# Performance work log

Hardware: AMD Instinct MI355X
Metric: run time of the kernel (lower is better)

The kernel has to match this reference:

```python
import jax, jax.numpy as jnp
import numpy as np
from jax import lax

BN_EPS = 1e-5
HEADS = 2


def dw_conv(x, w, stride, pad):
    # depthwise conv, NCHW, weight OIHW with I=1, groups=C
    return lax.conv_general_dilated(
        x, w, (stride, stride), [(pad, pad), (pad, pad)],
        dimension_numbers=('NCHW', 'OIHW', 'NCHW'),
        feature_group_count=x.shape[1])


def bn(x, g, b, m, v):
    inv = g * lax.rsqrt(v + BN_EPS)
    return (x - m[:, None, None]) * inv[:, None, None] + b[:, None, None]


def conv1x1(x, w, b):
    return jnp.einsum('bchw,oc->bohw', x, w) + b[:, None, None]


def setup_inputs() -> dict:
    key = jax.random.key(0)
    ks = jax.random.split(key, 20)
    B, C, H, W = 32, 128, 56, 56
    r = lambda i, shape, s=0.05: jax.random.normal(ks[i], shape, jnp.float32) * s
    return {
        'x': jax.random.normal(ks[0], (B, C, H, W), jnp.float32),
        'q_w': r(1, (C, C)), 'q_b': r(2, (C,)),
        'kv_w': r(3, (2 * C, C)), 'kv_b': r(4, (2 * C,)),
        'sr1_w': r(5, (C, 1, 4, 4), 0.2),
        'sr1_g': jax.random.uniform(ks[6], (C,), jnp.float32) + 0.5,
        'sr1_b': r(7, (C,)),
        'sr1_m': r(8, (C,)),
        'sr1_v': jax.random.uniform(ks[9], (C,), jnp.float32) + 0.5,
        'sr2_w': r(10, (C, 1, 1, 1), 0.5),
        'sr2_g': jax.random.uniform(ks[11], (C,), jnp.float32) + 0.5,
        'sr2_b': r(12, (C,)),
        'sr2_m': r(13, (C,)),
        'sr2_v': jax.random.uniform(ks[14], (C,), jnp.float32) + 0.5,
        'local_w': r(15, (C, 1, 3, 3), 0.2), 'local_b': r(16, (C,)),
    }


def reference(x, q_w, q_b, kv_w, kv_b,
              sr1_w, sr1_g, sr1_b, sr1_m, sr1_v,
              sr2_w, sr2_g, sr2_b, sr2_m, sr2_v,
              local_w, local_b):
    B, C, H, W = x.shape
    h = HEADS
    d = C // h
    scale = d ** -0.5

    # q projection: 1x1 conv -> [B, h, N, d]
    q = conv1x1(x, q_w, q_b)
    q = q.reshape(B, h, d, H * W).transpose(0, 1, 3, 2)

    # spatial reduction: depthwise strided conv + BN + ReLU, then depthwise 1x1 + BN
    kv = jax.nn.relu(bn(dw_conv(x, sr1_w, 4, 2), sr1_g, sr1_b, sr1_m, sr1_v))
    kv = bn(kv * sr2_w.reshape(C, 1, 1), sr2_g, sr2_b, sr2_m, sr2_v)

    # depthwise 3x3 local conv + residual
    kv = dw_conv(kv, local_w, 1, 1) + local_b[:, None, None] + kv

    # kv projection and split
    kvp = conv1x1(kv, kv_w, kv_b)
    k, v = jnp.split(kvp, 2, axis=1)
    Nk = k.shape[2] * k.shape[3]
    k = k.reshape(B, h, d, Nk)                       # [B,h,d,Nk]
    v = v.reshape(B, h, d, Nk).transpose(0, 1, 3, 2)  # [B,h,Nk,d]

    attn = jax.nn.softmax(jnp.einsum('bhnd,bhdm->bhnm', q, k) * scale, axis=-1)
    out = jnp.einsum('bhnm,bhmd->bhnd', attn, v)      # [B,h,N,d]
    return out.transpose(0, 1, 3, 2).reshape(B, C, H, W)
```

## Files before the change

kernel.cpp:

```cpp
#include <hip/hip_runtime.h>
#include <hip/hip_bf16.h>

#define B_    32
#define C_    128
#define H_    56
#define W_    56
#define N_    3136
#define HK_   15
#define NK_   225
#define D_    64

typedef __attribute__((ext_vector_type(8))) short bf16x8;
typedef __attribute__((ext_vector_type(4))) float f32x4;

__device__ __forceinline__ float b2f(unsigned short u) {
    union { float f; unsigned int i; } x;
    x.i = ((unsigned int)u) << 16;
    return x.f;
}
__device__ __forceinline__ unsigned short f2b(float f) {
    __hip_bfloat16 h = __float2bfloat16(f);
    return *(unsigned short*)&h;
}

__device__ __forceinline__ void gll16(const char* g, char* l) {
    __builtin_amdgcn_global_load_lds(
        (const __attribute__((address_space(1))) unsigned int*)g,
        (__attribute__((address_space(3))) unsigned int*)l,
        16, 0, 0);
}

__global__ __launch_bounds__(256) void srlocal_kernel(
        const float* __restrict__ x,
        const float* __restrict__ sr1_w, const float* __restrict__ sr1_g,
        const float* __restrict__ sr1_b, const float* __restrict__ sr1_m,
        const float* __restrict__ sr1_v, const float* __restrict__ sr2_w,
        const float* __restrict__ sr2_g, const float* __restrict__ sr2_b,
        const float* __restrict__ sr2_m, const float* __restrict__ sr2_v,
        const float* __restrict__ local_w, const float* __restrict__ local_b,
        float* __restrict__ kv2) {
    int bc = blockIdx.x;
    int c  = bc & (C_ - 1);
    int tid = threadIdx.x;
    __shared__ float xim[H_ * W_];
    __shared__ float kvt[HK_][HK_ + 1];

    const float* xp = x + (size_t)bc * (H_ * W_);
    for (int idx = tid; idx < (H_ * W_) / 4; idx += 256)
        ((float4*)xim)[idx] = ((const float4*)xp)[idx];
    __syncthreads();

    int p = tid;
    int oy = p / HK_, ox = p % HK_;
    if (p < NK_) {
        float s = 0.f;
#pragma unroll
        for (int ky = 0; ky < 4; ++ky) {
            int iy = oy * 4 - 2 + ky;
            if (iy < 0 || iy >= H_) continue;
#pragma unroll
            for (int kx = 0; kx < 4; ++kx) {
                int ix = ox * 4 - 2 + kx;
                if (ix < 0 || ix >= W_) continue;
                s += xim[iy * W_ + ix] * sr1_w[c * 16 + ky * 4 + kx];
            }
        }
        float inv1 = sr1_g[c] * rsqrtf(sr1_v[c] + 1e-5f);
        s = (s - sr1_m[c]) * inv1 + sr1_b[c];
        s = fmaxf(s, 0.f);
        s *= sr2_w[c];
        float inv2 = sr2_g[c] * rsqrtf(sr2_v[c] + 1e-5f);
        s = (s - sr2_m[c]) * inv2 + sr2_b[c];
        kvt[oy][ox] = s;
    }
    __syncthreads();
    if (p < NK_) {
        float v = kvt[oy][ox] + local_b[c];
#pragma unroll
        for (int dy = -1; dy <= 1; ++dy) {
            int yy = oy + dy;
            if (yy < 0 || yy >= HK_) continue;
#pragma unroll
            for (int dx = -1; dx <= 1; ++dx) {
                int xx = ox + dx;
                if (xx < 0 || xx >= HK_) continue;
                v += kvt[yy][xx] * local_w[c * 9 + (dy + 1) * 3 + (dx + 1)];
            }
        }
        kv2[(size_t)bc * NK_ + p] = v;
    }
}

__global__ __launch_bounds__(256) void wprep_kernel(
        const float* __restrict__ q_w, const float* __restrict__ q_b,
        const float* __restrict__ kv_w, const float* __restrict__ kv_b,
        unsigned short* __restrict__ wkq_sw, unsigned short* __restrict__ wv_sw,
        float* __restrict__ kwb, float* __restrict__ wb, float* __restrict__ qkb) {
    int bx = blockIdx.x;
    int h  = bx >> 3, cg = bx & 7;
    int tid = threadIdx.x;
    __shared__ float wk_s[64][128];
    __shared__ float wq_s[64][16];

    for (int idx = tid; idx < 64 * 128; idx += 256)
        wk_s[idx >> 7][idx & 127] = kv_w[(size_t)(h * 64 + (idx >> 7)) * 128 + (idx & 127)];
    for (int idx = tid; idx < 64 * 16; idx += 256)
        wq_s[idx >> 4][idx & 15] = q_w[(size_t)(h * 64 + (idx >> 4)) * 128 + cg * 16 + (idx & 15)];
    __syncthreads();

    {
        int cl = tid >> 4;
        int c  = cg * 16 + cl;
        int cp0 = (tid & 15) * 8;
        float acc[8];
#pragma unroll
        for (int i = 0; i < 8; ++i) acc[i] = 0.f;
        for (int e = 0; e < 64; ++e) {
            float wqv = wq_s[e][cl];
#pragma unroll
            for (int i = 0; i < 8; ++i) acc[i] += wqv * wk_s[e][cp0 + i];
        }
        char* base = (char*)wkq_sw + (size_t)h * 32768 + (size_t)c * 256;
        ushort4 u0, u1;
        u0.x = f2b(acc[0] * 0.125f); u0.y = f2b(acc[1] * 0.125f);
        u0.z = f2b(acc[2] * 0.125f); u0.w = f2b(acc[3] * 0.125f);
        u1.x = f2b(acc[4] * 0.125f); u1.y = f2b(acc[5] * 0.125f);
        u1.z = f2b(acc[6] * 0.125f); u1.w = f2b(acc[7] * 0.125f);
        int sw = (c & 7) << 4;
        *(ushort4*)(base + ((cp0 * 2) ^ sw)) = u0;
        *(ushort4*)(base + ((cp0 * 2 + 8) ^ sw)) = u1;
    }
    if (tid < 16) {
        int cl = tid, c = cg * 16 + cl;
        float s = 0.f;
        for (int e = 0; e < 64; ++e) s += kv_b[h * 64 + e] * wq_s[e][cl];
        kwb[h * 128 + c] = s * 0.125f;
    }
    if (cg == 0) {
        if (tid < 128) {
            float s = 0.f;
            for (int e = 0; e < 64; ++e) s += q_b[h * 64 + e] * wk_s[e][tid];
            wb[h * 128 + tid] = s * 0.125f;
        }
        if (tid == 0) {
            float s = 0.f;
            for (int e = 0; e < 64; ++e) s += q_b[h * 64 + e] * kv_b[h * 64 + e];
            qkb[h] = s * 0.125f;
        }
    }
    if (cg == 1) {
        for (int idx = tid; idx < 64 * 128; idx += 256) {
            int e = idx >> 7, cp = idx & 127;
            unsigned short val = f2b(kv_w[(size_t)(128 + h * 64 + e) * 128 + cp]);
            *(unsigned short*)((char*)wv_sw + (size_t)h * 16384 + (size_t)e * 256 +
                               (((cp * 2) ^ ((e & 7) << 4)))) = val;
        }
    }
}

#define L2B(r, cb) ((r) * 256 + ((cb) ^ (((r) & 7) << 4)))
__global__ __launch_bounds__(256, 2) void kvw_kernel(
        const float* __restrict__ kv2,
        const float* __restrict__ kv_b,
        const unsigned short* __restrict__ wkq_sw,
        const unsigned short* __restrict__ wv_sw,
        const float* __restrict__ kwb,
        const float* __restrict__ wb,
        const float* __restrict__ qkb,
        unsigned short* __restrict__ kw,
        float* __restrict__ bias_s,
        unsigned short* __restrict__ vbuf) {
    int b = blockIdx.x, h = blockIdx.y, mh = blockIdx.z;
    int bh = b * 2 + h;
    int m0 = mh * 64;
    int tid = threadIdx.x;
    int lo = tid & 15, hi = (tid >> 4) & 3, wid = tid >> 6;

    __shared__ char K2[16384];
    __shared__ char WQ[32768];
    __shared__ char WV[16384];

    {
        const char* srcQ = (const char*)wkq_sw + (size_t)h * 32768 + tid * 16;
        char* dstQ = WQ + wid * 1024;
#pragma unroll
        for (int i = 0; i < 8; ++i) gll16(srcQ + i * 4096, dstQ + i * 4096);
        const char* srcV = (const char*)wv_sw + (size_t)h * 16384 + tid * 16;
        char* dstV = WV + wid * 1024;
#pragma unroll
        for (int i = 0; i < 4; ++i) gll16(srcV + i * 4096, dstV + i * 4096);
    }
    {
        int j = tid & 63;
        int mg = m0 + j;
        bool val = (mg < NK_);
#pragma unroll
        for (int it = 0; it < 8; ++it) {
            int c0 = (tid >> 6) * 4 + it * 16;
            ushort4 u;
            if (val) {
                const float* kp = kv2 + ((size_t)b * 128 + c0) * NK_ + mg;
                u.x = f2b(kp[0]);
                u.y = f2b(kp[NK_]);
                u.z = f2b(kp[2 * NK_]);
                u.w = f2b(kp[3 * NK_]);
            } else { u.x = 0; u.y = 0; u.z = 0; u.w = 0; }
            *(ushort4*)(K2 + L2B(j, c0 * 2)) = u;
        }
    }
    __syncthreads();

    bf16x8 aq[4];
#pragma unroll
    for (int ks = 0; ks < 4; ++ks)
        aq[ks] = *(const bf16x8*)(K2 + L2B(wid * 16 + lo, ks * 64 + hi * 16));

    char* kwB = (char*)kw + (size_t)bh * 65536;
#pragma unroll
    for (int ct = 0; ct < 8; ++ct) {
        f32x4 acc = {0.f, 0.f, 0.f, 0.f};
#pragma unroll
        for (int ks = 0; ks < 4; ++ks) {
            bf16x8 bq = *(const bf16x8*)(WQ + L2B(ct * 16 + lo, ks * 64 + hi * 16));
            acc = __builtin_amdgcn_mfma_f32_16x16x32_bf16(aq[ks], bq, acc, 0, 0, 0);
        }
        int c = ct * 16 + lo;
        float kb = kwb[h * 128 + c];
#pragma unroll
        for (int r = 0; r < 4; ++r) {
            int mg = m0 + wid * 16 + hi * 4 + r;
            *(unsigned short*)(kwB + (size_t)mg * 256 + (((c * 2) ^ ((mg & 7) << 4)))) =
                f2b(acc[r] + kb);
        }
    }

    char* vB = (char*)vbuf + (size_t)bh * 32768;
#pragma unroll
    for (int et = 0; et < 4; ++et) {
        f32x4 acc = {0.f, 0.f, 0.f, 0.f};
#pragma unroll
        for (int ks = 0; ks < 4; ++ks) {
            bf16x8 bv = *(const bf16x8*)(WV + L2B(et * 16 + lo, ks * 64 + hi * 16));
            acc = __builtin_amdgcn_mfma_f32_16x16x32_bf16(aq[ks], bv, acc, 0, 0, 0);
        }
        int e = et * 16 + lo;
        float vb = kv_b[128 + h * 64 + e];
#pragma unroll
        for (int r = 0; r < 4; ++r) {
            int mg = m0 + wid * 16 + hi * 4 + r;
            *(unsigned short*)(vB + (size_t)e * 512 + (((mg * 2) ^ ((e & 7) << 4)))) =
                f2b(acc[r] + vb);
        }
    }

    if (tid < 64) {
        int mg = m0 + tid;
        float s;
        if (mg >= NK_) s = -1e30f;
        else {
            s = qkb[h];
            for (int i = 0; i < 128; ++i) {
                int cp = (i + (tid & 7) * 16) & 127;
                s += b2f(*(const unsigned short*)(K2 + L2B(tid, cp * 2))) * wb[h * 128 + cp];
            }
        }
        bias_s[(size_t)bh * 256 + mg] = s;
    }
}

#define XTB(j, c) ((j) * 256 + (((c) * 2) ^ (((j) & 15) << 4)))
#define PSB(j, m) ((j) * 512 + (((m) * 2) ^ (((j) & 15) << 4)))
#define KWB(rl, cb) ((rl) * 256 + ((cb) ^ (((rl) & 7) << 4)))
#define CVB(e, cb)  ((e) * 512 + ((cb) ^ (((e) & 7) << 4)))

__global__ __launch_bounds__(256, 2) void attn_kernel(
        const float* __restrict__ x,
        const unsigned short* __restrict__ kw,
        const float* __restrict__ bias_s,
        const unsigned short* __restrict__ vbuf,
        float* __restrict__ out) {
    int flat = blockIdx.x;
    int xcd  = flat & 7;
    int idx  = flat >> 3;
    int g    = idx / 49;
    int jt   = idx % 49;
    int bh   = g * 8 + xcd;
    int bb   = bh >> 1;
    int h    = bh & 1;
    int n0   = jt * 64;
    int tid = threadIdx.x;
    int lo  = tid & 15;
    int hi  = (tid >> 4) & 3;
    int wid = tid >> 6;
    int jw  = wid * 16;

    __shared__ char A[32768];
    __shared__ char Bt[2][8192];
    __shared__ char Cv[32768];

    const char* kwG = (const char*)kw + (size_t)bh * 65536;
    const char* vG  = (const char*)vbuf + (size_t)bh * 32768;

#pragma unroll
    for (int it = 0; it < 8; ++it) {
        int j  = tid & 63;
        int c0 = (tid >> 6) * 4 + it * 16;
        const float* xp = x + ((size_t)bb * 128 + c0) * N_ + n0 + j;
        ushort4 u;
        u.x = f2b(xp[0]);
        u.y = f2b(xp[(size_t)N_]);
        u.z = f2b(xp[2 * (size_t)N_]);
        u.w = f2b(xp[3 * (size_t)N_]);
        *(ushort4*)(A + XTB(j, c0)) = u;
    }
    float bs[16];
    {
        const float* bsp = bias_s + (size_t)bh * 256;
#pragma unroll
        for (int mt = 0; mt < 16; ++mt) bs[mt] = bsp[mt * 16 + lo];
    }
    {
        const char* s0 = kwG + tid * 16;
        char* d0 = Bt[0] + wid * 1024;
        gll16(s0, d0); gll16(s0 + 4096, d0 + 4096);
        const char* s1 = kwG + 8192 + tid * 16;
        char* d1 = Bt[1] + wid * 1024;
        gll16(s1, d1); gll16(s1 + 4096, d1 + 4096);
        const char* sc = vG + tid * 16;
        char* dc = Cv + wid * 1024;
#pragma unroll
        for (int i = 0; i < 8; ++i) gll16(sc + i * 4096, dc + i * 4096);
    }
    asm volatile("s_waitcnt vmcnt(10) lgkmcnt(0)" ::: "memory");
    __builtin_amdgcn_s_barrier();
    __builtin_amdgcn_sched_barrier(0);

    bf16x8 aq[4];
#pragma unroll
    for (int ks = 0; ks < 4; ++ks)
        aq[ks] = *(const bf16x8*)(A + XTB(jw + lo, ks * 32 + hi * 8));

    f32x4 s[16];
#pragma unroll
    for (int t = 0; t < 8; ++t) {
#pragma unroll
        for (int ml = 0; ml < 2; ++ml) {
            f32x4 acc = {0.f, 0.f, 0.f, 0.f};
#pragma unroll
            for (int ks = 0; ks < 4; ++ks) {
                bf16x8 bk = *(const bf16x8*)(Bt[t & 1] + KWB(ml * 16 + lo, ks * 64 + hi * 16));
                acc = __builtin_amdgcn_mfma_f32_16x16x32_bf16(aq[ks], bk, acc, 0, 0, 0);
            }
            s[t * 2 + ml] = acc;
        }
        if (t < 6) {
            __builtin_amdgcn_s_barrier();
            const char* sn = kwG + (t + 2) * 8192 + tid * 16;
            char* dn = Bt[t & 1] + wid * 1024;
            gll16(sn, dn); gll16(sn + 4096, dn + 4096);
        }
        if (t < 7) {
            if (t == 0)      asm volatile("s_waitcnt vmcnt(10)" ::: "memory");
            else if (t < 6)  asm volatile("s_waitcnt vmcnt(2)" ::: "memory");
            else             asm volatile("s_waitcnt vmcnt(0)" ::: "memory");
            __builtin_amdgcn_s_barrier();
            __builtin_amdgcn_sched_barrier(0);
        }
    }

#pragma unroll
    for (int mt = 0; mt < 16; ++mt) {
#pragma unroll
        for (int r = 0; r < 4; ++r) s[mt][r] += bs[mt];
    }
    float mx[4];
#pragma unroll
    for (int r = 0; r < 4; ++r) {
        float m0v = s[0][r];
#pragma unroll
        for (int mt = 1; mt < 16; ++mt) m0v = fmaxf(m0v, s[mt][r]);
        mx[r] = m0v;
    }
#pragma unroll
    for (int d = 1; d < 16; d <<= 1) {
#pragma unroll
        for (int r = 0; r < 4; ++r) mx[r] = fmaxf(mx[r], __shfl_xor(mx[r], d));
    }
    float sm[4] = {0.f, 0.f, 0.f, 0.f};
#pragma unroll
    for (int mt = 0; mt < 16; ++mt) {
#pragma unroll
        for (int r = 0; r < 4; ++r) {
            float pe = __expf(s[mt][r] - mx[r]);
            s[mt][r] = pe;
            sm[r] += pe;
        }
    }
#pragma unroll
    for (int d = 1; d < 16; d <<= 1) {
#pragma unroll
        for (int r = 0; r < 4; ++r) sm[r] += __shfl_xor(sm[r], d);
    }
    float rinv[4];
#pragma unroll
    for (int r = 0; r < 4; ++r) rinv[r] = 1.f / sm[r];

#pragma unroll
    for (int mt = 0; mt < 16; ++mt) {
#pragma unroll
        for (int r = 0; r < 4; ++r)
            *(unsigned short*)(A + PSB(jw + hi * 4 + r, mt * 16 + lo)) =
                f2b(s[mt][r] * rinv[r]);
    }

    bf16x8 bp[8];
#pragma unroll
    for (int ks = 0; ks < 8; ++ks)
        bp[ks] = *(const bf16x8*)(A + PSB(jw + lo, ks * 32 + hi * 8));
#pragma unroll
    for (int et = 0; et < 4; ++et) {
        f32x4 acc = {0.f, 0.f, 0.f, 0.f};
#pragma unroll
        for (int ks = 0; ks < 8; ++ks) {
            bf16x8 av = *(const bf16x8*)(Cv + CVB(et * 16 + lo, ks * 64 + hi * 16));
            acc = __builtin_amdgcn_mfma_f32_16x16x32_bf16(av, bp[ks], acc, 0, 0, 0);
        }
        int e = et * 16 + hi * 4;
#pragma unroll
        for (int r = 0; r < 4; ++r)
            out[((size_t)bb * 128 + h * 64 + e + r) * N_ + n0 + jw + lo] = acc[r];
    }
}

extern "C" void kernel_launch(void* const* d_in, const int* in_sizes, int n_in,
                              void* d_out, int out_size, void* d_ws, size_t ws_size,
                              hipStream_t stream) {
    const float* x       = (const float*)d_in[0];
    const float* q_w     = (const float*)d_in[1];
    const float* q_b     = (const float*)d_in[2];
    const float* kv_w    = (const float*)d_in[3];
    const float* kv_b    = (const float*)d_in[4];
    const float* sr1_w   = (const float*)d_in[5];
    const float* sr1_g   = (const float*)d_in[6];
    const float* sr1_b   = (const float*)d_in[7];
    const float* sr1_m   = (const float*)d_in[8];
    const float* sr1_v   = (const float*)d_in[9];
    const float* sr2_w   = (const float*)d_in[10];
    const float* sr2_g   = (const float*)d_in[11];
    const float* sr2_b   = (const float*)d_in[12];
    const float* sr2_m   = (const float*)d_in[13];
    const float* sr2_v   = (const float*)d_in[14];
    const float* local_w = (const float*)d_in[15];
    const float* local_b = (const float*)d_in[16];

    char* ws = (char*)d_ws;
    float* kv2              = (float*)(ws + 0);
    unsigned short* wkq_sw  = (unsigned short*)(ws + 3686400);
    unsigned short* wv_sw   = (unsigned short*)(ws + 3751936);
    unsigned short* kw      = (unsigned short*)(ws + 3784704);
    unsigned short* vbuf    = (unsigned short*)(ws + 7979008);
    float* bias_s           = (float*)(ws + 10076160);
    float* kwb              = (float*)(ws + 10141696);
    float* wb               = (float*)(ws + 10142720);
    float* qkb              = (float*)(ws + 10143744);

    wprep_kernel<<<16, 256, 0, stream>>>(q_w, q_b, kv_w, kv_b,
                                         wkq_sw, wv_sw, kwb, wb, qkb);
    srlocal_kernel<<<B_ * C_, 256, 0, stream>>>(
        x, sr1_w, sr1_g, sr1_b, sr1_m, sr1_v,
        sr2_w, sr2_g, sr2_b, sr2_m, sr2_v, local_w, local_b, kv2);
    kvw_kernel<<<dim3(B_, 2, 4), 256, 0, stream>>>(
        kv2, kv_b, wkq_sw, wv_sw, kwb, wb, qkb, kw, bias_s, vbuf);
    attn_kernel<<<3136, 256, 0, stream>>>(
        x, kw, bias_s, vbuf, (float*)d_out);
}
```

Measured before the change: 103.3 us.

## Merge weight-prep into spatial-reduction kernel and slim attention LDS for 3 blocks/CU

Folds the weight-prep kernel into the spatial-reduction kernel as extra blocks, removing one launch. The attention kernel cuts its LDS footprint by reusing the Q staging buffer for the K tiles, and raises the launch bound from 2 to 3 blocks per CU. It also swaps MFMA operand order so softmax reductions become two cross-lane shuffles, and builds the P operand via register shuffles instead of an LDS round trip. Normalization is deferred to the output store, the all-padding 16th key tile is skipped, and V/bias loads are issued early. This brings more register pressure and a more complex shuffle-based data path.

```diff
diff --git a/kernel.cpp b/kernel.cpp
--- a/kernel.cpp
+++ b/kernel.cpp
@@ -22,6 +22,9 @@
     __hip_bfloat16 h = __float2bfloat16(f);
     return *(unsigned short*)&h;
 }
+__device__ __forceinline__ unsigned int pkbf(float a, float b) {
+    return (unsigned int)f2b(a) | ((unsigned int)f2b(b) << 16);
+}
 
 __device__ __forceinline__ void gll16(const char* g, char* l) {
     __builtin_amdgcn_global_load_lds(
@@ -30,7 +33,7 @@
         16, 0, 0);
 }
 
-__global__ __launch_bounds__(256) void srlocal_kernel(
+__global__ __launch_bounds__(256) void prep_kernel(
         const float* __restrict__ x,
         const float* __restrict__ sr1_w, const float* __restrict__ sr1_g,
         const float* __restrict__ sr1_b, const float* __restrict__ sr1_m,
@@ -38,16 +41,82 @@
         const float* __restrict__ sr2_g, const float* __restrict__ sr2_b,
         const float* __restrict__ sr2_m, const float* __restrict__ sr2_v,
         const float* __restrict__ local_w, const float* __restrict__ local_b,
-        float* __restrict__ kv2) {
+        const float* __restrict__ q_w, const float* __restrict__ q_b,
+        const float* __restrict__ kv_w, const float* __restrict__ kv_b,
+        float* __restrict__ kv2,
+        unsigned short* __restrict__ wkq_sw, unsigned short* __restrict__ wv_sw,
+        float* __restrict__ kwb, float* __restrict__ wb, float* __restrict__ qkb) {
+    int tid = threadIdx.x;
+    __shared__ union {
+        struct { float xim[H_ * W_]; float kvt[HK_][HK_ + 1]; } sr;
+        float wq[64][16];
+    } U;
+
+    if (blockIdx.x >= (unsigned)(B_ * C_)) {
+        int bx = blockIdx.x - B_ * C_;
+        int h  = bx >> 3, cg = bx & 7;
+        for (int idx = tid; idx < 64 * 16; idx += 256)
+            U.wq[idx >> 4][idx & 15] =
+                q_w[(size_t)(h * 64 + (idx >> 4)) * 128 + cg * 16 + (idx & 15)];
+        __syncthreads();
+        {
+            int cl = tid >> 4;
+            int c  = cg * 16 + cl;
+            int cp0 = (tid & 15) * 8;
+            float acc[8];
+#pragma unroll
+            for (int i = 0; i < 8; ++i) acc[i] = 0.f;
+            for (int e = 0; e < 64; ++e) {
+                float wqv = U.wq[e][cl];
+                const float* wkrow = kv_w + (size_t)(h * 64 + e) * 128 + cp0;
+#pragma unroll
+                for (int i = 0; i < 8; ++i) acc[i] += wqv * wkrow[i];
+            }
+            char* base = (char*)wkq_sw + (size_t)h * 32768 + (size_t)c * 256;
+            ushort4 u0, u1;
+            u0.x = f2b(acc[0] * 0.125f); u0.y = f2b(acc[1] * 0.125f);
+            u0.z = f2b(acc[2] * 0.125f); u0.w = f2b(acc[3] * 0.125f);
+            u1.x = f2b(acc[4] * 0.125f); u1.y = f2b(acc[5] * 0.125f);
+            u1.z = f2b(acc[6] * 0.125f); u1.w = f2b(acc[7] * 0.125f);
+            int sw = (c & 7) << 4;
+            *(ushort4*)(base + ((cp0 * 2) ^ sw)) = u0;
+            *(ushort4*)(base + ((cp0 * 2 + 8) ^ sw)) = u1;
+        }
+        if (tid < 16) {
+            int cl = tid, c = cg * 16 + cl;
+            float s = 0.f;
+            for (int e = 0; e < 64; ++e) s += kv_b[h * 64 + e] * U.wq[e][cl];
+            kwb[h * 128 + c] = s * 0.125f;
+        }
+        if (cg == 0) {
+            if (tid < 128) {
+                float s = 0.f;
+                for (int e = 0; e < 64; ++e)
+                    s += q_b[h * 64 + e] * kv_w[(size_t)(h * 64 + e) * 128 + tid];
+                wb[h * 128 + tid] = s * 0.125f;
+            }
+            if (tid == 0) {
+                float s = 0.f;
+                for (int e = 0; e < 64; ++e) s += q_b[h * 64 + e] * kv_b[h * 64 + e];
+                qkb[h] = s * 0.125f;
+            }
+        }
+        if (cg == 1) {
+            for (int idx = tid; idx < 64 * 128; idx += 256) {
+                int e = idx >> 7, cp = idx & 127;
+                unsigned short val = f2b(kv_w[(size_t)(128 + h * 64 + e) * 128 + cp]);
+                *(unsigned short*)((char*)wv_sw + (size_t)h * 16384 + (size_t)e * 256 +
+                                   (((cp * 2) ^ ((e & 7) << 4)))) = val;
+            }
+        }
+        return;
+    }
+
     int bc = blockIdx.x;
     int c  = bc & (C_ - 1);
-    int tid = threadIdx.x;
-    __shared__ float xim[H_ * W_];
-    __shared__ float kvt[HK_][HK_ + 1];
-
     const float* xp = x + (size_t)bc * (H_ * W_);
     for (int idx = tid; idx < (H_ * W_) / 4; idx += 256)
-        ((float4*)xim)[idx] = ((const float4*)xp)[idx];
+        ((float4*)U.sr.xim)[idx] = ((const float4*)xp)[idx];
     __syncthreads();
 
     int p = tid;
@@ -62,7 +131,7 @@
             for (int kx = 0; kx < 4; ++kx) {
                 int ix = ox * 4 - 2 + kx;
                 if (ix < 0 || ix >= W_) continue;
-                s += xim[iy * W_ + ix] * sr1_w[c * 16 + ky * 4 + kx];
+                s += U.sr.xim[iy * W_ + ix] * sr1_w[c * 16 + ky * 4 + kx];
             }
         }
         float inv1 = sr1_g[c] * rsqrtf(sr1_v[c] + 1e-5f);
@@ -71,11 +140,11 @@
         s *= sr2_w[c];
         float inv2 = sr2_g[c] * rsqrtf(sr2_v[c] + 1e-5f);
         s = (s - sr2_m[c]) * inv2 + sr2_b[c];
-        kvt[oy][ox] = s;
+        U.sr.kvt[oy][ox] = s;
     }
     __syncthreads();
     if (p < NK_) {
-        float v = kvt[oy][ox] + local_b[c];
+        float v = U.sr.kvt[oy][ox] + local_b[c];
 #pragma unroll
         for (int dy = -1; dy <= 1; ++dy) {
             int yy = oy + dy;
@@ -84,77 +153,10 @@
             for (int dx = -1; dx <= 1; ++dx) {
                 int xx = ox + dx;
                 if (xx < 0 || xx >= HK_) continue;
-                v += kvt[yy][xx] * local_w[c * 9 + (dy + 1) * 3 + (dx + 1)];
+                v += U.sr.kvt[yy][xx] * local_w[c * 9 + (dy + 1) * 3 + (dx + 1)];
             }
         }
         kv2[(size_t)bc * NK_ + p] = v;
-    }
-}
-
-__global__ __launch_bounds__(256) void wprep_kernel(
-        const float* __restrict__ q_w, const float* __restrict__ q_b,
-        const float* __restrict__ kv_w, const float* __restrict__ kv_b,
-        unsigned short* __restrict__ wkq_sw, unsigned short* __restrict__ wv_sw,
-        float* __restrict__ kwb, float* __restrict__ wb, float* __restrict__ qkb) {
-    int bx = blockIdx.x;
-    int h  = bx >> 3, cg = bx & 7;
-    int tid = threadIdx.x;
-    __shared__ float wk_s[64][128];
-    __shared__ float wq_s[64][16];
-
-    for (int idx = tid; idx < 64 * 128; idx += 256)
-        wk_s[idx >> 7][idx & 127] = kv_w[(size_t)(h * 64 + (idx >> 7)) * 128 + (idx & 127)];
-    for (int idx = tid; idx < 64 * 16; idx += 256)
-        wq_s[idx >> 4][idx & 15] = q_w[(size_t)(h * 64 + (idx >> 4)) * 128 + cg * 16 + (idx & 15)];
-    __syncthreads();
-
-    {
-        int cl = tid >> 4;
-        int c  = cg * 16 + cl;
-        int cp0 = (tid & 15) * 8;
-        float acc[8];
-#pragma unroll
-        for (int i = 0; i < 8; ++i) acc[i] = 0.f;
-        for (int e = 0; e < 64; ++e) {
-            float wqv = wq_s[e][cl];
-#pragma unroll
-            for (int i = 0; i < 8; ++i) acc[i] += wqv * wk_s[e][cp0 + i];
-        }
-        char* base = (char*)wkq_sw + (size_t)h * 32768 + (size_t)c * 256;
-        ushort4 u0, u1;
-        u0.x = f2b(acc[0] * 0.125f); u0.y = f2b(acc[1] * 0.125f);
-        u0.z = f2b(acc[2] * 0.125f); u0.w = f2b(acc[3] * 0.125f);
-        u1.x = f2b(acc[4] * 0.125f); u1.y = f2b(acc[5] * 0.125f);
-        u1.z = f2b(acc[6] * 0.125f); u1.w = f2b(acc[7] * 0.125f);
-        int sw = (c & 7) << 4;
-        *(ushort4*)(base + ((cp0 * 2) ^ sw)) = u0;
-        *(ushort4*)(base + ((cp0 * 2 + 8) ^ sw)) = u1;
-    }
-    if (tid < 16) {
-        int cl = tid, c = cg * 16 + cl;
-        float s = 0.f;
-        for (int e = 0; e < 64; ++e) s += kv_b[h * 64 + e] * wq_s[e][cl];
-        kwb[h * 128 + c] = s * 0.125f;
-    }
-    if (cg == 0) {
-        if (tid < 128) {
-            float s = 0.f;
-            for (int e = 0; e < 64; ++e) s += q_b[h * 64 + e] * wk_s[e][tid];
-            wb[h * 128 + tid] = s * 0.125f;
-        }
-        if (tid == 0) {
-            float s = 0.f;
-            for (int e = 0; e < 64; ++e) s += q_b[h * 64 + e] * kv_b[h * 64 + e];
-            qkb[h] = s * 0.125f;
-        }
-    }
-    if (cg == 1) {
-        for (int idx = tid; idx < 64 * 128; idx += 256) {
-            int e = idx >> 7, cp = idx & 127;
-            unsigned short val = f2b(kv_w[(size_t)(128 + h * 64 + e) * 128 + cp]);
-            *(unsigned short*)((char*)wv_sw + (size_t)h * 16384 + (size_t)e * 256 +
-                               (((cp * 2) ^ ((e & 7) << 4)))) = val;
-        }
     }
 }
 
@@ -269,11 +271,10 @@
 }
 
 #define XTB(j, c) ((j) * 256 + (((c) * 2) ^ (((j) & 15) << 4)))
-#define PSB(j, m) ((j) * 512 + (((m) * 2) ^ (((j) & 15) << 4)))
 #define KWB(rl, cb) ((rl) * 256 + ((cb) ^ (((rl) & 7) << 4)))
 #define CVB(e, cb)  ((e) * 512 + ((cb) ^ (((e) & 7) << 4)))
 
-__global__ __launch_bounds__(256, 2) void attn_kernel(
+__global__ __launch_bounds__(256, 3) void attn_kernel(
         const float* __restrict__ x,
         const unsigned short* __restrict__ kw,
         const float* __restrict__ bias_s,
@@ -294,13 +295,20 @@
     int wid = tid >> 6;
     int jw  = wid * 16;
 
-    __shared__ char A[32768];
-    __shared__ char Bt[2][8192];
-    __shared__ char Cv[32768];
+    __shared__ char LA[16384];
+    __shared__ char LC[32768];
+    __shared__ float LBIAS[256];
 
     const char* kwG = (const char*)kw + (size_t)bh * 65536;
     const char* vG  = (const char*)vbuf + (size_t)bh * 32768;
 
+    {
+#pragma unroll
+        for (int i = 0; i < 8; ++i)
+            gll16(vG + i * 4096 + tid * 16, LC + i * 4096 + wid * 1024);
+        if (wid == 0)
+            gll16((const char*)(bias_s + (size_t)bh * 256) + tid * 16, (char*)LBIAS);
+    }
 #pragma unroll
     for (int it = 0; it < 8; ++it) {
         int j  = tid & 63;
@@ -311,124 +319,137 @@
         u.y = f2b(xp[(size_t)N_]);
         u.z = f2b(xp[2 * (size_t)N_]);
         u.w = f2b(xp[3 * (size_t)N_]);
-        *(ushort4*)(A + XTB(j, c0)) = u;
-    }
-    float bs[16];
-    {
-        const float* bsp = bias_s + (size_t)bh * 256;
-#pragma unroll
-        for (int mt = 0; mt < 16; ++mt) bs[mt] = bsp[mt * 16 + lo];
-    }
+        *(ushort4*)(LA + XTB(j, c0)) = u;
+    }
+    asm volatile("s_waitcnt lgkmcnt(0)" ::: "memory");
+    __builtin_amdgcn_s_barrier();
+
+    bf16x8 aq[4];
+#pragma unroll
+    for (int ks = 0; ks < 4; ++ks)
+        aq[ks] = *(const bf16x8*)(LA + XTB(jw + lo, ks * 32 + hi * 8));
+    asm volatile("s_waitcnt lgkmcnt(0)" ::: "memory");
+    __builtin_amdgcn_s_barrier();
+    __builtin_amdgcn_sched_barrier(0);
+
     {
         const char* s0 = kwG + tid * 16;
-        char* d0 = Bt[0] + wid * 1024;
+        char* d0 = LA + wid * 1024;
         gll16(s0, d0); gll16(s0 + 4096, d0 + 4096);
         const char* s1 = kwG + 8192 + tid * 16;
-        char* d1 = Bt[1] + wid * 1024;
+        char* d1 = LA + 8192 + wid * 1024;
         gll16(s1, d1); gll16(s1 + 4096, d1 + 4096);
-        const char* sc = vG + tid * 16;
-        char* dc = Cv + wid * 1024;
-#pragma unroll
-        for (int i = 0; i < 8; ++i) gll16(sc + i * 4096, dc + i * 4096);
-    }
-    asm volatile("s_waitcnt vmcnt(10) lgkmcnt(0)" ::: "memory");
+    }
+    asm volatile("s_waitcnt vmcnt(2)" ::: "memory");
     __builtin_amdgcn_s_barrier();
     __builtin_amdgcn_sched_barrier(0);
 
-    bf16x8 aq[4];
-#pragma unroll
-    for (int ks = 0; ks < 4; ++ks)
-        aq[ks] = *(const bf16x8*)(A + XTB(jw + lo, ks * 32 + hi * 8));
-
-    f32x4 s[16];
+    f32x4 s[15];
 #pragma unroll
     for (int t = 0; t < 8; ++t) {
+        char* Bt = LA + (t & 1) * 8192;
 #pragma unroll
         for (int ml = 0; ml < 2; ++ml) {
+            int mt = t * 2 + ml;
+            if (mt >= 15) continue;
             f32x4 acc = {0.f, 0.f, 0.f, 0.f};
 #pragma unroll
             for (int ks = 0; ks < 4; ++ks) {
-                bf16x8 bk = *(const bf16x8*)(Bt[t & 1] + KWB(ml * 16 + lo, ks * 64 + hi * 16));
-                acc = __builtin_amdgcn_mfma_f32_16x16x32_bf16(aq[ks], bk, acc, 0, 0, 0);
-            }
-            s[t * 2 + ml] = acc;
+                bf16x8 bk = *(const bf16x8*)(Bt + KWB(ml * 16 + lo, ks * 64 + hi * 16));
+                acc = __builtin_amdgcn_mfma_f32_16x16x32_bf16(bk, aq[ks], acc, 0, 0, 0);
+            }
+            s[mt] = acc;
         }
         if (t < 6) {
             __builtin_amdgcn_s_barrier();
             const char* sn = kwG + (t + 2) * 8192 + tid * 16;
-            char* dn = Bt[t & 1] + wid * 1024;
+            char* dn = LA + (t & 1) * 8192 + wid * 1024;
             gll16(sn, dn); gll16(sn + 4096, dn + 4096);
         }
         if (t < 7) {
-            if (t == 0)      asm volatile("s_waitcnt vmcnt(10)" ::: "memory");
-            else if (t < 6)  asm volatile("s_waitcnt vmcnt(2)" ::: "memory");
-            else             asm volatile("s_waitcnt vmcnt(0)" ::: "memory");
+            if (t < 6) asm volatile("s_waitcnt vmcnt(2)" ::: "memory");
+            else       asm volatile("s_waitcnt vmcnt(0)" ::: "memory");
             __builtin_amdgcn_s_barrier();
             __builtin_amdgcn_sched_barrier(0);
         }
     }
 
 #pragma unroll
-    for (int mt = 0; mt < 16; ++mt) {
-#pragma unroll
-        for (int r = 0; r < 4; ++r) s[mt][r] += bs[mt];
-    }
-    float mx[4];
-#pragma unroll
-    for (int r = 0; r < 4; ++r) {
-        float m0v = s[0][r];
-#pragma unroll
-        for (int mt = 1; mt < 16; ++mt) m0v = fmaxf(m0v, s[mt][r]);
-        mx[r] = m0v;
-    }
-#pragma unroll
-    for (int d = 1; d < 16; d <<= 1) {
-#pragma unroll
-        for (int r = 0; r < 4; ++r) mx[r] = fmaxf(mx[r], __shfl_xor(mx[r], d));
-    }
-    float sm[4] = {0.f, 0.f, 0.f, 0.f};
-#pragma unroll
-    for (int mt = 0; mt < 16; ++mt) {
+    for (int mt = 0; mt < 15; ++mt) {
+        f32x4 bv = *(const f32x4*)&LBIAS[mt * 16 + hi * 4];
+#pragma unroll
+        for (int r = 0; r < 4; ++r) s[mt][r] += bv[r];
+    }
+
+    float mxv = s[0][0];
+#pragma unroll
+    for (int mt = 0; mt < 15; ++mt) {
+#pragma unroll
+        for (int r = 0; r < 4; ++r) mxv = fmaxf(mxv, s[mt][r]);
+    }
+    mxv = fmaxf(mxv, __shfl_xor(mxv, 16));
+    mxv = fmaxf(mxv, __shfl_xor(mxv, 32));
+    float smv = 0.f;
+#pragma unroll
+    for (int mt = 0; mt < 15; ++mt) {
 #pragma unroll
         for (int r = 0; r < 4; ++r) {
-            float pe = __expf(s[mt][r] - mx[r]);
+            float pe = __expf(s[mt][r] - mxv);
             s[mt][r] = pe;
-            sm[r] += pe;
-        }
-    }
-#pragma unroll
-    for (int d = 1; d < 16; d <<= 1) {
-#pragma unroll
-        for (int r = 0; r < 4; ++r) sm[r] += __shfl_xor(sm[r], d);
-    }
-    float rinv[4];
-#pragma unroll
-    for (int r = 0; r < 4; ++r) rinv[r] = 1.f / sm[r];
-
-#pragma unroll
-    for (int mt = 0; mt < 16; ++mt) {
-#pragma unroll
-        for (int r = 0; r < 4; ++r)
-            *(unsigned short*)(A + PSB(jw + hi * 4 + r, mt * 16 + lo)) =
-                f2b(s[mt][r] * rinv[r]);
-    }
+            smv += pe;
+        }
+    }
+    smv += __shfl_xor(smv, 16);
+    smv += __shfl_xor(smv, 32);
+    float rinv = 1.f / smv;
 
     bf16x8 bp[8];
-#pragma unroll
-    for (int ks = 0; ks < 8; ++ks)
-        bp[ks] = *(const bf16x8*)(A + PSB(jw + lo, ks * 32 + hi * 8));
+    int sA = lo + (hi & 1) * 32;
+    int sB = sA + 16;
+    bool lowm = (hi < 2);
+#pragma unroll
+    for (int ks = 0; ks < 8; ++ks) {
+        int t0 = 2 * ks, t1 = 2 * ks + 1;
+        unsigned int a0 = pkbf(s[t0][0], s[t0][1]);
+        unsigned int a1 = pkbf(s[t0][2], s[t0][3]);
+        unsigned int r0A = (unsigned int)__shfl((int)a0, sA);
+        unsigned int r1A = (unsigned int)__shfl((int)a1, sA);
+        unsigned int r0B = (unsigned int)__shfl((int)a0, sB);
+        unsigned int r1B = (unsigned int)__shfl((int)a1, sB);
+        unsigned int dw0, dw1, dw2, dw3;
+        if (ks < 7) {
+            unsigned int b0 = pkbf(s[t1][0], s[t1][1]);
+            unsigned int b1 = pkbf(s[t1][2], s[t1][3]);
+            unsigned int q0A = (unsigned int)__shfl((int)b0, sA);
+            unsigned int q1A = (unsigned int)__shfl((int)b1, sA);
+            unsigned int q0B = (unsigned int)__shfl((int)b0, sB);
+            unsigned int q1B = (unsigned int)__shfl((int)b1, sB);
+            dw0 = lowm ? r0A : q0A;
+            dw1 = lowm ? r1A : q1A;
+            dw2 = lowm ? r0B : q0B;
+            dw3 = lowm ? r1B : q1B;
+        } else {
+            dw0 = lowm ? r0A : 0u;
+            dw1 = lowm ? r1A : 0u;
+            dw2 = lowm ? r0B : 0u;
+            dw3 = lowm ? r1B : 0u;
+        }
+        uint4 d4 = {dw0, dw1, dw2, dw3};
+        bp[ks] = *(bf16x8*)&d4;
+    }
+
 #pragma unroll
     for (int et = 0; et < 4; ++et) {
         f32x4 acc = {0.f, 0.f, 0.f, 0.f};
 #pragma unroll
         for (int ks = 0; ks < 8; ++ks) {
-            bf16x8 av = *(const bf16x8*)(Cv + CVB(et * 16 + lo, ks * 64 + hi * 16));
+            bf16x8 av = *(const bf16x8*)(LC + CVB(et * 16 + lo, ks * 64 + hi * 16));
             acc = __builtin_amdgcn_mfma_f32_16x16x32_bf16(av, bp[ks], acc, 0, 0, 0);
         }
         int e = et * 16 + hi * 4;
 #pragma unroll
         for (int r = 0; r < 4; ++r)
-            out[((size_t)bb * 128 + h * 64 + e + r) * N_ + n0 + jw + lo] = acc[r];
+            out[((size_t)bb * 128 + h * 64 + e + r) * N_ + n0 + jw + lo] = acc[r] * rinv;
     }
 }
 
@@ -464,11 +485,11 @@
     float* wb               = (float*)(ws + 10142720);
     float* qkb              = (float*)(ws + 10143744);
 
-    wprep_kernel<<<16, 256, 0, stream>>>(q_w, q_b, kv_w, kv_b,
-                                         wkq_sw, wv_sw, kwb, wb, qkb);
-    srlocal_kernel<<<B_ * C_, 256, 0, stream>>>(
+    prep_kernel<<<B_ * C_ + 16, 256, 0, stream>>>(
         x, sr1_w, sr1_g, sr1_b, sr1_m, sr1_v,
-        sr2_w, sr2_g, sr2_b, sr2_m, sr2_v, local_w, local_b, kv2);
+        sr2_w, sr2_g, sr2_b, sr2_m, sr2_v, local_w, local_b,
+        q_w, q_b, kv_w, kv_b,
+        kv2, wkq_sw, wv_sw, kwb, wb, qkb);
     kvw_kernel<<<dim3(B_, 2, 4), 256, 0, stream>>>(
         kv2, kv_b, wkq_sw, wv_sw, kwb, wb, qkb, kw, bias_s, vbuf);
     attn_kernel<<<3136, 256, 0, stream>>>(
```

Result: faster. 89.49 us (-13.4%).
